# Optimization experiments

Hardware: AMD Instinct MI355X
Metric: run time of the kernel (lower is better)

## Reference

```python
import jax, jax.numpy as jnp
import numpy as np

B, GH, GW = 8, 32, 32
S = GH * GW            # 1024
HIDDEN = 512
D = 64                 # head_dim
NUM_HOPS = 2
EPS = 1e-6


def setup_inputs() -> dict:
    key = jax.random.key(0)
    ks = jax.random.split(key, 8)

    def init(k, shape, std):
        return (jax.random.normal(k, shape) * std).astype(jnp.float32)

    x = jax.random.normal(ks[0], (B, S, HIDDEN), dtype=jnp.float32)
    Wq = init(ks[1], (D, HIDDEN), HIDDEN ** -0.5)
    Wk = init(ks[2], (D, HIDDEN), HIDDEN ** -0.5)
    Wv = init(ks[3], (D, HIDDEN), HIDDEN ** -0.5)
    bias_table = init(ks[4], (2 * GH - 1, 2 * GW - 1), 0.02)
    fusion_w = jnp.ones((NUM_HOPS, 3), dtype=jnp.float32)
    fusion_b = jnp.zeros((NUM_HOPS,), dtype=jnp.float32)
    hop_W = init(ks[5], (NUM_HOPS, D, D), D ** -0.5)
    gate_W = init(ks[6], (NUM_HOPS, HIDDEN), HIDDEN ** -0.5)
    gate_b = jnp.zeros((NUM_HOPS,), dtype=jnp.float32)
    out_W = init(ks[7], (HIDDEN, D), D ** -0.5)
    temperature = jnp.ones((1,), dtype=jnp.float32)

    # relative position index [S, S] (buffer, constant)
    coords = np.stack(np.meshgrid(np.arange(GH), np.arange(GW), indexing='ij')).reshape(2, -1)
    rel = coords[:, :, None] - coords[:, None, :]
    rel[0] += GH - 1
    rel[1] += GW - 1
    rel_idx = jnp.asarray(rel[0] * (2 * GW - 1) + rel[1], dtype=jnp.int32)

    return dict(x=x, Wq=Wq, Wk=Wk, Wv=Wv, bias_table=bias_table,
                fusion_w=fusion_w, fusion_b=fusion_b, hop_W=hop_W,
                gate_W=gate_W, gate_b=gate_b, out_W=out_W,
                temperature=temperature, rel_idx=rel_idx)


def _rotate_half(u):
    d = u.shape[-1] // 2
    return jnp.concatenate([-u[..., d:], u[..., :d]], axis=-1)


def _prob_log(p):
    p = jnp.clip(p, EPS, 1.0 - EPS)
    return jnp.log(p / (1.0 - p + EPS))


def _mat_exp(M, h):
    R = M
    for _ in range(h - 1):
        R = jnp.matmul(R, M)
    return R


def _row_norm(M):
    return M / (jnp.sum(M, axis=-1, keepdims=True) + EPS)


def reference(x, Wq, Wk, Wv, bias_table, fusion_w, fusion_b, hop_W,
              gate_W, gate_b, out_W, temperature, rel_idx):
    b, s, hdim = x.shape
    d = Wq.shape[0]
    n_hops = hop_W.shape[0]
    scale = jnp.sqrt(jnp.float32(d))

    Q = jnp.einsum('bsh,dh->bsd', x, Wq)
    K = jnp.einsum('bsh,dh->bsd', x, Wk)
    V = jnp.einsum('bsh,dh->bsd', x, Wv)

    # RoPE (cached cos/sin are deterministic functions of S, D)
    inv_freq = 1.0 / (10000.0 ** (jnp.arange(0, d, 2, dtype=jnp.float32) / d))
    t = jnp.arange(s, dtype=jnp.float32)
    emb = jnp.concatenate([jnp.outer(t, inv_freq)] * 2, axis=-1)  # [S, D]
    cos, sin = jnp.cos(emb), jnp.sin(emb)
    Q = Q * cos + _rotate_half(Q) * sin
    K = K * cos + _rotate_half(K) * sin

    pb = bias_table.reshape(-1)[rel_idx]  # [S, S]
    scores = (jnp.einsum('bsd,btd->bst', Q, K) / scale + pb[None])
    scores = scores / jnp.clip(temperature, 0.1, None)
    A = jax.nn.softmax(scores, axis=-1)  # [B, S, S]

    A_T = jnp.swapaxes(A, -1, -2)
    AAt = jnp.matmul(A, A_T)
    AtA = jnp.matmul(A_T, A)

    hop_outs = []
    for hop in range(n_hops):
        h = hop + 1
        A_seq = _row_norm(_mat_exp(A, h))
        A_co = _row_norm(_mat_exp(AAt, h))
        A_sp = _row_norm(_mat_exp(AtA, h))
        fused_logit = (fusion_b[hop]
                       + fusion_w[hop, 0] * _prob_log(A_seq)
                       + fusion_w[hop, 1] * _prob_log(A_co)
                       + fusion_w[hop, 2] * _prob_log(A_sp))
        fused = _row_norm(jax.nn.sigmoid(fused_logit))
        hop_v = jnp.einsum('bsd,ed->bse', V, hop_W[hop])
        hop_outs.append(jnp.matmul(fused, hop_v))  # [B, S, D]

    gate = jax.nn.softmax(jnp.einsum('bsh,gh->bsg', x, gate_W) + gate_b, axis=-1)
    combined = sum(hop_outs[i] * gate[..., i:i + 1] for i in range(n_hops))
    return jnp.einsum('bsd,hd->bsh', combined, out_W)
```

## Files before the change

kernel.cpp:

```cpp
#include <hip/hip_runtime.h>
#include <hip/hip_bf16.h>

#define BB 8
#define SS 1024
#define HH 512
#define DD 64

typedef unsigned short u16;
typedef short v8s __attribute__((ext_vector_type(8)));
typedef float v4f __attribute__((ext_vector_type(4)));

__device__ __forceinline__ float bf2f(u16 u) {
    union { unsigned int i; float f; } v; v.i = ((unsigned int)u) << 16; return v.f;
}
__device__ __forceinline__ u16 f2bf(float f) {
    union { float f; unsigned int i; } v; v.f = f;
    unsigned int u = v.i;
    unsigned int r = u + 0x7fffu + ((u >> 16) & 1u);
    return (u16)(r >> 16);
}

__device__ __forceinline__ void gload16(const u16* g, u16* l) {
    __builtin_amdgcn_global_load_lds(
        (const __attribute__((address_space(1))) void*)g,
        (__attribute__((address_space(3))) void*)l,
        16, 0, 0);
}

__device__ __forceinline__ void tile_1024(
    const u16* __restrict__ Xb, const u16* __restrict__ Yb,
    u16* __restrict__ Cd, int tm, int tn, u16* Xs, u16* Ys, int mirror)
{
    int t = threadIdx.x, lane = t & 63, w = t >> 6;
    int wm = (w & 1) << 6, wn = (w >> 1) << 6;
    int fr = lane & 15, q = lane >> 4, m7 = fr & 7;
    int subrow = lane >> 3, cch = (lane & 7) ^ subrow;

    const u16* xg[4]; const u16* yg[4]; u16* xl[4]; u16* yl[4];
    #pragma unroll
    for (int i = 0; i < 4; i++) {
        int r = i * 32 + w * 8 + subrow;
        xg[i] = Xb + (long)(tm + r) * 1024 + cch * 8;
        yg[i] = Yb + (long)(tn + r) * 1024 + cch * 8;
        xl[i] = Xs + (i * 32 + w * 8) * 64;
        yl[i] = Ys + (i * 32 + w * 8) * 64;
    }

    v4f acc[4][4];
    #pragma unroll
    for (int i = 0; i < 4; i++)
        #pragma unroll
        for (int j = 0; j < 4; j++) {
            acc[i][j][0] = 0.f; acc[i][j][1] = 0.f; acc[i][j][2] = 0.f; acc[i][j][3] = 0.f;
        }

    for (int k0 = 0; k0 < 1024; k0 += 64) {
        __syncthreads();
        #pragma unroll
        for (int i = 0; i < 4; i++) { gload16(xg[i] + k0, xl[i]); gload16(yg[i] + k0, yl[i]); }
        __syncthreads();
        v8s af[2][4], bfr[2][4];
        #pragma unroll
        for (int h = 0; h < 2; h++) {
            int ca = (((h << 2) + q) ^ m7) << 3;
            #pragma unroll
            for (int s = 0; s < 4; s++) {
                af[h][s]  = *(const v8s*)(Xs + (wm + s * 16 + fr) * 64 + ca);
                bfr[h][s] = *(const v8s*)(Ys + (wn + s * 16 + fr) * 64 + ca);
            }
        }
        #pragma unroll
        for (int h = 0; h < 2; h++)
            #pragma unroll
            for (int i = 0; i < 4; i++)
                #pragma unroll
                for (int j = 0; j < 4; j++)
                    acc[i][j] = __builtin_amdgcn_mfma_f32_16x16x32_bf16(af[h][i], bfr[h][j], acc[i][j], 0, 0, 0);
    }
    #pragma unroll
    for (int i = 0; i < 4; i++) {
        int rowb = tm + wm + i * 16 + q * 4;
        #pragma unroll
        for (int j = 0; j < 4; j++) {
            int col = tn + wn + j * 16 + fr;
            ushort4 pv;
            pv.x = f2bf(acc[i][j][0]); pv.y = f2bf(acc[i][j][1]);
            pv.z = f2bf(acc[i][j][2]); pv.w = f2bf(acc[i][j][3]);
            #pragma unroll
            for (int r = 0; r < 4; r++)
                Cd[(long)(rowb + r) * 1024 + col] = ((u16*)&pv)[r];
            if (mirror)
                *(ushort4*)(Cd + (long)col * 1024 + rowb) = pv;
        }
    }
}

__device__ __forceinline__ void tile_k64(
    const u16* __restrict__ Xrows, const u16* __restrict__ Yrows,
    void* __restrict__ Cd, int crs, int cf32, u16* Xs, u16* Ys)
{
    int t = threadIdx.x, lane = t & 63, w = t >> 6;
    int wm = (w & 1) << 6, wn = (w >> 1) << 6;
    int fr = lane & 15, q = lane >> 4, m7 = fr & 7;
    int subrow = lane >> 3, cch = (lane & 7) ^ subrow;

    #pragma unroll
    for (int i = 0; i < 4; i++) {
        int r = i * 32 + w * 8 + subrow;
        gload16(Xrows + (long)r * 64 + cch * 8, Xs + (i * 32 + w * 8) * 64);
        gload16(Yrows + (long)r * 64 + cch * 8, Ys + (i * 32 + w * 8) * 64);
    }
    __syncthreads();

    v4f acc[4][4];
    #pragma unroll
    for (int i = 0; i < 4; i++)
        #pragma unroll
        for (int j = 0; j < 4; j++) {
            acc[i][j][0] = 0.f; acc[i][j][1] = 0.f; acc[i][j][2] = 0.f; acc[i][j][3] = 0.f;
        }
    v8s af[2][4], bfr[2][4];
    #pragma unroll
    for (int h = 0; h < 2; h++) {
        int ca = (((h << 2) + q) ^ m7) << 3;
        #pragma unroll
        for (int s = 0; s < 4; s++) {
            af[h][s]  = *(const v8s*)(Xs + (wm + s * 16 + fr) * 64 + ca);
            bfr[h][s] = *(const v8s*)(Ys + (wn + s * 16 + fr) * 64 + ca);
        }
    }
    #pragma unroll
    for (int h = 0; h < 2; h++)
        #pragma unroll
        for (int i = 0; i < 4; i++)
            #pragma unroll
            for (int j = 0; j < 4; j++)
                acc[i][j] = __builtin_amdgcn_mfma_f32_16x16x32_bf16(af[h][i], bfr[h][j], acc[i][j], 0, 0, 0);
    #pragma unroll
    for (int i = 0; i < 4; i++) {
        int rowb = wm + i * 16 + q * 4;
        #pragma unroll
        for (int j = 0; j < 4; j++) {
            int col = wn + j * 16 + fr;
            #pragma unroll
            for (int r = 0; r < 4; r++) {
                long o = (long)(rowb + r) * crs + col;
                if (cf32) ((float*)Cd)[o] = acc[i][j][r];
                else      ((u16*)Cd)[o] = f2bf(acc[i][j][r]);
            }
        }
    }
}

__device__ __forceinline__ void hop_tile(
    const u16* __restrict__ Fb, const u16* __restrict__ Hb,
    int y, int tmt, float* __restrict__ Pd, u16* Fs, u16* Hs)
{
    int tm = tmt * 128, kb = y * 256;
    int t = threadIdx.x, lane = t & 63, w = t >> 6;
    int fr = lane & 15, q = lane >> 4, m7 = fr & 7;
    int subrow = lane >> 3, cch = (lane & 7) ^ subrow;

    const u16* fg[4]; u16* fl[4]; const u16* hg[2]; u16* hl[2];
    #pragma unroll
    for (int i = 0; i < 4; i++) {
        int r = i * 32 + w * 8 + subrow;
        fg[i] = Fb + (long)(tm + r) * 1024 + cch * 8;
        fl[i] = Fs + (i * 32 + w * 8) * 64;
    }
    #pragma unroll
    for (int i = 0; i < 2; i++) {
        int r = i * 32 + w * 8 + subrow;
        hg[i] = Hb + (long)r * 1024 + cch * 8;
        hl[i] = Hs + (i * 32 + w * 8) * 64;
    }

    v4f acc[2][4];
    #pragma unroll
    for (int i = 0; i < 2; i++)
        #pragma unroll
        for (int j = 0; j < 4; j++) {
            acc[i][j][0] = 0.f; acc[i][j][1] = 0.f; acc[i][j][2] = 0.f; acc[i][j][3] = 0.f;
        }

    for (int k0 = kb; k0 < kb + 256; k0 += 64) {
        __syncthreads();
        #pragma unroll
        for (int i = 0; i < 4; i++) gload16(fg[i] + k0, fl[i]);
        #pragma unroll
        for (int i = 0; i < 2; i++) gload16(hg[i] + k0, hl[i]);
        __syncthreads();
        v8s af[2][2], bfr[2][4];
        #pragma unroll
        for (int h = 0; h < 2; h++) {
            int ca = (((h << 2) + q) ^ m7) << 3;
            #pragma unroll
            for (int s = 0; s < 2; s++)
                af[h][s] = *(const v8s*)(Fs + (w * 32 + s * 16 + fr) * 64 + ca);
            #pragma unroll
            for (int s = 0; s < 4; s++)
                bfr[h][s] = *(const v8s*)(Hs + (s * 16 + fr) * 64 + ca);
        }
        #pragma unroll
        for (int h = 0; h < 2; h++)
            #pragma unroll
            for (int i = 0; i < 2; i++)
                #pragma unroll
                for (int j = 0; j < 4; j++)
                    acc[i][j] = __builtin_amdgcn_mfma_f32_16x16x32_bf16(af[h][i], bfr[h][j], acc[i][j], 0, 0, 0);
    }
    #pragma unroll
    for (int i = 0; i < 2; i++) {
        int rowb = tm + w * 32 + i * 16 + q * 4;
        #pragma unroll
        for (int j = 0; j < 4; j++) {
            int col = j * 16 + fr;
            #pragma unroll
            for (int r = 0; r < 4; r++)
                Pd[(long)(rowb + r) * 64 + col] = acc[i][j][r];
        }
    }
}

__device__ __forceinline__ void fused_row(
    const u16* __restrict__ r1, const u16* __restrict__ r2, const u16* __restrict__ r3,
    float w0, float w1, float w2, float b0, u16* __restrict__ Frow, int lane)
{
    int base = lane << 4;
    union U { uint4 v; u16 s[8]; };
    U a[2], b[2], c[2];
    a[0].v = *(const uint4*)(r1 + base); a[1].v = *(const uint4*)(r1 + base + 8);
    b[0].v = *(const uint4*)(r2 + base); b[1].v = *(const uint4*)(r2 + base + 8);
    c[0].v = *(const uint4*)(r3 + base); c[1].v = *(const uint4*)(r3 + base + 8);
    float m1[16], m2[16], m3[16];
    float s1 = 0.f, s2 = 0.f, s3 = 0.f;
    #pragma unroll
    for (int h = 0; h < 2; h++)
        #pragma unroll
        for (int e = 0; e < 8; e++) {
            int k = h * 8 + e;
            m1[k] = bf2f(a[h].s[e]); m2[k] = bf2f(b[h].s[e]); m3[k] = bf2f(c[h].s[e]);
            s1 += m1[k]; s2 += m2[k]; s3 += m3[k];
        }
    #pragma unroll
    for (int o = 1; o < 64; o <<= 1) {
        s1 += __shfl_xor(s1, o); s2 += __shfl_xor(s2, o); s3 += __shfl_xor(s3, o);
    }
    float i1 = 1.f / (s1 + 1e-6f), i2 = 1.f / (s2 + 1e-6f), i3 = 1.f / (s3 + 1e-6f);
    float sig[16];
    float ssum = 0.f;
    #pragma unroll
    for (int k = 0; k < 16; k++) {
        float p1 = fminf(fmaxf(m1[k] * i1, 1e-6f), 1.0f - 1e-6f);
        float p2 = fminf(fmaxf(m2[k] * i2, 1e-6f), 1.0f - 1e-6f);
        float p3 = fminf(fmaxf(m3[k] * i3, 1e-6f), 1.0f - 1e-6f);
        float l1 = __logf(p1 / (1.0f - p1 + 1e-6f));
        float l2 = __logf(p2 / (1.0f - p2 + 1e-6f));
        float l3 = __logf(p3 / (1.0f - p3 + 1e-6f));
        float lg = b0 + w0 * l1 + w1 * l2 + w2 * l3;
        float sg = 1.0f / (1.0f + __expf(-lg));
        sig[k] = sg; ssum += sg;
    }
    #pragma unroll
    for (int o = 1; o < 64; o <<= 1) ssum += __shfl_xor(ssum, o);
    float inv = 1.0f / (ssum + 1e-6f);
    U o0, o1;
    #pragma unroll
    for (int e = 0; e < 8; e++) { o0.s[e] = f2bf(sig[e] * inv); o1.s[e] = f2bf(sig[8 + e] * inv); }
    *(uint4*)(Frow + base) = o0.v;
    *(uint4*)(Frow + base + 8) = o1.v;
}

__global__ __launch_bounds__(256) void gemm_link1(
    const u16* __restrict__ A, const u16* __restrict__ AT,
    u16* __restrict__ AAt, u16* __restrict__ AtA, u16* __restrict__ A2)
{
    __shared__ u16 Xs[128 * 64];
    __shared__ u16 Ys[128 * 64];
    const long SSq = (long)SS * SS;
    int b = blockIdx.x & 7;
    int job = blockIdx.x >> 3;
    const u16* Xb; const u16* Yb; u16* Cd;
    int ti, tj, mir;
    if (job < 72) {
        int tt = job < 36 ? job : job - 36;
        ti = 0;
        while (tt >= 8 - ti) { tt -= 8 - ti; ti++; }
        tj = ti + tt;
        mir = (ti != tj);
        if (job < 36) { Xb = A  + b * SSq; Yb = Xb; Cd = AAt + b * SSq; }
        else          { Xb = AT + b * SSq; Yb = Xb; Cd = AtA + b * SSq; }
    } else {
        int jj = job - 72;
        ti = jj >> 3; tj = jj & 7; mir = 0;
        Xb = A + b * SSq; Yb = AT + b * SSq; Cd = A2 + b * SSq;
    }
    tile_1024(Xb, Yb, Cd, ti * 128, tj * 128, Xs, Ys, mir);
}

__global__ __launch_bounds__(256) void k_link2_fused0(
    const u16* __restrict__ AAt, const u16* __restrict__ AtA,
    u16* __restrict__ AAt2, u16* __restrict__ AtA2,
    const u16* __restrict__ A, const float* __restrict__ fw,
    const float* __restrict__ fbv, u16* __restrict__ F0)
{
    __shared__ u16 Xs[128 * 64];
    __shared__ u16 Ys[128 * 64];
    const long SSq = (long)SS * SS;
    int bx = blockIdx.x;
    if (bx < 576) {
        int z = bx & 15;
        int tt = bx >> 4, ti = 0;
        while (tt >= 8 - ti) { tt -= 8 - ti; ti++; }
        int tj = ti + tt;
        const u16* Xb = (z < 8 ? AAt : AtA) + (long)(z & 7) * SSq;
        u16* Cd = (z < 8 ? AAt2 : AtA2) + (long)(z & 7) * SSq;
        tile_1024(Xb, Xb, Cd, ti * 128, tj * 128, Xs, Ys, ti != tj);
    } else {
        int lane = threadIdx.x & 63, w = threadIdx.x >> 6;
        float w0 = fw[0], w1 = fw[1], w2 = fw[2], b0 = fbv[0];
        long row = (long)(bx - 576) * 4 + w;
        fused_row(A + row * 1024, AAt + row * 1024, AtA + row * 1024,
                  w0, w1, w2, b0, F0 + row * 1024, lane);
    }
}

__global__ __launch_bounds__(256) void k_hop0_fused1(
    const u16* __restrict__ F0, const u16* __restrict__ hopVT,
    float* __restrict__ Pa, float* __restrict__ Pb,
    const u16* __restrict__ A2, const u16* __restrict__ AAt2,
    const u16* __restrict__ AtA2, const float* __restrict__ fw,
    const float* __restrict__ fbv, u16* __restrict__ F1)
{
    __shared__ u16 Fs[128 * 64];
    __shared__ u16 Hs[64 * 64];
    const long SSq = (long)SS * SS;
    int bx = blockIdx.x;
    if (bx < 256) {
        int y = bx >> 6, rest = bx & 63;
        int tmt = rest >> 3, b = rest & 7;
        float* Pd = (y < 2 ? Pa + (long)y * 16 * 65536 : Pb + (long)(y - 2) * 16 * 65536)
                    + (long)b * 65536;
        hop_tile(F0 + (long)b * SSq, hopVT + (long)b * 65536, y, tmt, Pd, Fs, Hs);
    } else {
        int lane = threadIdx.x & 63, w = threadIdx.x >> 6;
        float w0 = fw[3], w1 = fw[4], w2 = fw[5], b0 = fbv[1];
        long row = (long)(bx - 256) * 4 + w;
        fused_row(A2 + row * 1024, AAt2 + row * 1024, AtA2 + row * 1024,
                  w0, w1, w2, b0, F1 + row * 1024, lane);
    }
}

__global__ __launch_bounds__(256) void gemm_hop1(
    const u16* __restrict__ F1, const u16* __restrict__ hopVT,
    float* __restrict__ Pa, float* __restrict__ Pb)
{
    __shared__ u16 Fs[128 * 64];
    __shared__ u16 Hs[64 * 64];
    const long SSq = (long)SS * SS;
    int j = blockIdx.x;
    int y = j >> 6, rest = j & 63;
    int tmt = rest >> 3, b = rest & 7;
    float* Pd = (y < 2 ? Pa + (long)y * 16 * 65536 : Pb + (long)(y - 2) * 16 * 65536)
                + (long)(8 + b) * 65536;
    hop_tile(F1 + (long)b * SSq, hopVT + (long)(8 + b) * 65536, y, tmt, Pd, Fs, Hs);
}

__global__ __launch_bounds__(256) void gemm_nt(
    const u16* __restrict__ X, long sx,
    const u16* __restrict__ Y, long sy,
    void* __restrict__ Cv, long sc,
    int M, int N, int K, int cf32)
{
    __shared__ u16 Xs[128 * 64];
    __shared__ u16 Ys[128 * 64];
    const u16* Xb = X + (long)blockIdx.z * sx;
    const u16* Yb = Y + (long)blockIdx.z * sy;
    int tm = blockIdx.x * 128, tn = blockIdx.y * 128;
    int t = threadIdx.x, lane = t & 63, w = t >> 6;
    int wm = (w & 1) << 6, wn = (w >> 1) << 6;
    int fr = lane & 15, q = lane >> 4, m7 = fr & 7;
    int subrow = lane >> 3, cch = (lane & 7) ^ subrow;

    const u16* xg[4]; const u16* yg[4]; u16* xl[4]; u16* yl[4];
    #pragma unroll
    for (int i = 0; i < 4; i++) {
        int r = i * 32 + w * 8 + subrow;
        xg[i] = Xb + (long)(tm + r) * K + cch * 8;
        yg[i] = Yb + (long)(tn + r) * K + cch * 8;
        xl[i] = Xs + (i * 32 + w * 8) * 64;
        yl[i] = Ys + (i * 32 + w * 8) * 64;
    }

    v4f acc[4][4];
    #pragma unroll
    for (int i = 0; i < 4; i++)
        #pragma unroll
        for (int j = 0; j < 4; j++) {
            acc[i][j][0] = 0.f; acc[i][j][1] = 0.f; acc[i][j][2] = 0.f; acc[i][j][3] = 0.f;
        }

    for (int k0 = 0; k0 < K; k0 += 64) {
        __syncthreads();
        #pragma unroll
        for (int i = 0; i < 4; i++) { gload16(xg[i] + k0, xl[i]); gload16(yg[i] + k0, yl[i]); }
        __syncthreads();
        v8s af[2][4], bfr[2][4];
        #pragma unroll
        for (int h = 0; h < 2; h++) {
            int ca = (((h << 2) + q) ^ m7) << 3;
            #pragma unroll
            for (int s = 0; s < 4; s++) {
                af[h][s]  = *(const v8s*)(Xs + (wm + s * 16 + fr) * 64 + ca);
                bfr[h][s] = *(const v8s*)(Ys + (wn + s * 16 + fr) * 64 + ca);
            }
        }
        #pragma unroll
        for (int h = 0; h < 2; h++)
            #pragma unroll
            for (int i = 0; i < 4; i++)
                #pragma unroll
                for (int j = 0; j < 4; j++)
                    acc[i][j] = __builtin_amdgcn_mfma_f32_16x16x32_bf16(af[h][i], bfr[h][j], acc[i][j], 0, 0, 0);
    }
    long cb = (long)blockIdx.z * sc;
    #pragma unroll
    for (int i = 0; i < 4; i++) {
        int rowb = tm + wm + i * 16 + q * 4;
        #pragma unroll
        for (int j = 0; j < 4; j++) {
            int col = tn + wn + j * 16 + fr;
            #pragma unroll
            for (int r = 0; r < 4; r++) {
                long o = cb + (long)(rowb + r) * N + col;
                if (cf32) ((float*)Cv)[o] = acc[i][j][r];
                else      ((u16*)Cv)[o] = f2bf(acc[i][j][r]);
            }
        }
    }
}

__global__ __launch_bounds__(256) void k_proj_rope(
    const u16* __restrict__ xb, const u16* __restrict__ wpack,
    const float* __restrict__ gateb, const float2* __restrict__ ropetab,
    u16* __restrict__ Qb, u16* __restrict__ Kb, u16* __restrict__ Vb,
    float* __restrict__ gate)
{
    __shared__ u16 Xs[128 * 64];
    __shared__ u16 Ys[128 * 64];
    int tm = blockIdx.x * 128, tn = blockIdx.y * 128;
    int t = threadIdx.x, lane = t & 63, w = t >> 6;
    int wm = (w & 1) << 6, wn = (w >> 1) << 6;
    int fr = lane & 15, q = lane >> 4, m7 = fr & 7;
    int subrow = lane >> 3, cch = (lane & 7) ^ subrow;

    const u16* xg[4]; const u16* yg[4]; u16* xl[4]; u16* yl[4];
    #pragma unroll
    for (int i = 0; i < 4; i++) {
        int r = i * 32 + w * 8 + subrow;
        xg[i] = xb + (long)(tm + r) * 512 + cch * 8;
        yg[i] = wpack + (long)(tn + r) * 512 + cch * 8;
        xl[i] = Xs + (i * 32 + w * 8) * 64;
        yl[i] = Ys + (i * 32 + w * 8) * 64;
    }

    v4f acc[4][4];
    #pragma unroll
    for (int i = 0; i < 4; i++)
        #pragma unroll
        for (int j = 0; j < 4; j++) {
            acc[i][j][0] = 0.f; acc[i][j][1] = 0.f; acc[i][j][2] = 0.f; acc[i][j][3] = 0.f;
        }

    for (int k0 = 0; k0 < 512; k0 += 64) {
        __syncthreads();
        #pragma unroll
        for (int i = 0; i < 4; i++) { gload16(xg[i] + k0, xl[i]); gload16(yg[i] + k0, yl[i]); }
        __syncthreads();
        v8s af[2][4], bfr[2][4];
        #pragma unroll
        for (int h = 0; h < 2; h++) {
            int ca = (((h << 2) + q) ^ m7) << 3;
            #pragma unroll
            for (int s = 0; s < 4; s++) {
                af[h][s]  = *(const v8s*)(Xs + (wm + s * 16 + fr) * 64 + ca);
                bfr[h][s] = *(const v8s*)(Ys + (wn + s * 16 + fr) * 64 + ca);
            }
        }
        #pragma unroll
        for (int h = 0; h < 2; h++)
            #pragma unroll
            for (int i = 0; i < 4; i++)
                #pragma unroll
                for (int j = 0; j < 4; j++)
                    acc[i][j] = __builtin_amdgcn_mfma_f32_16x16x32_bf16(af[h][i], bfr[h][j], acc[i][j], 0, 0, 0);
    }

    if (blockIdx.y == 0) {
        u16* dst = wn ? Kb : Qb;
        #pragma unroll
        for (int i = 0; i < 4; i++) {
            #pragma unroll
            for (int r = 0; r < 4; r++) {
                int row = tm + wm + i * 16 + q * 4 + r;
                int spos = row & (SS - 1);
                float2 t0 = ropetab[spos * 32 + fr];
                float2 t1 = ropetab[spos * 32 + 16 + fr];
                #pragma unroll
                for (int j = 0; j < 4; j++) {
                    float v = acc[i][j][r], p = acc[i][j ^ 2][r];
                    float cs = (j & 1) ? t1.x : t0.x;
                    float sn = (j & 1) ? t1.y : t0.y;
                    float o = (j & 2) ? (v * cs + p * sn) : (v * cs - p * sn);
                    dst[(long)row * 64 + j * 16 + fr] = f2bf(o);
                }
            }
        }
    } else if (wn == 0) {
        #pragma unroll
        for (int i = 0; i < 4; i++)
            #pragma unroll
            for (int j = 0; j < 4; j++)
                #pragma unroll
                for (int r = 0; r < 4; r++) {
                    int row = tm + wm + i * 16 + q * 4 + r;
                    Vb[(long)row * 64 + j * 16 + fr] = f2bf(acc[i][j][r]);
                }
    } else {
        float gb = gateb[fr & 1];
        #pragma unroll
        for (int i = 0; i < 4; i++)
            #pragma unroll
            for (int r = 0; r < 4; r++) {
                int row = tm + wm + i * 16 + q * 4 + r;
                float g = acc[i][0][r] + gb;
                float go = __shfl_xor(g, 1);
                float m = fmaxf(g, go);
                float e = __expf(g - m), eo = __expf(go - m);
                if (fr < 2) gate[(long)row * 2 + fr] = e / (e + eo);
            }
    }
}

__global__ __launch_bounds__(256) void k_qk_hopv(
    const u16* __restrict__ Qb, const u16* __restrict__ Kb,
    const u16* __restrict__ Vb, const u16* __restrict__ hopWb,
    float* __restrict__ scores, u16* __restrict__ hopvC)
{
    __shared__ u16 Xs[128 * 64];
    __shared__ u16 Ys[128 * 64];
    const long SSq = (long)SS * SS;
    const long SD = (long)SS * DD;
    int bx = blockIdx.x;
    if (bx < 512) {
        int z = bx & 7;
        int tt = bx >> 3;
        int tm = (tt >> 3) * 128, tn = (tt & 7) * 128;
        tile_k64(Qb + z * SD + (long)tm * 64, Kb + z * SD + (long)tn * 64,
                 scores + z * SSq + (long)tm * 1024 + tn, 1024, 1, Xs, Ys);
    } else {
        int tm = (bx - 512) * 128;
        tile_k64(Vb + (long)tm * 64, hopWb,
                 hopvC + (long)tm * 128, 128, 0, Xs, Ys);
    }
}

__global__ __launch_bounds__(256) void k_sm_hvt(
    const float* __restrict__ scores, const float* __restrict__ btab,
    const float* __restrict__ temp, u16* __restrict__ A,
    u16* __restrict__ AT,
    const u16* __restrict__ hopvC, u16* __restrict__ hopVT)
{
    __shared__ __align__(16) float smf[3969];
    __shared__ __align__(8) u16 Atile[4096];
    int bx = blockIdx.x;
    int t = threadIdx.x;
    if (bx < 2048) {
        for (int i = t; i < 3969; i += 256) smf[i] = btab[i];
        __syncthreads();
        int lane = t & 63, w = t >> 6;
        long row = (long)bx * 4 + w;
        int i = (int)(row & 1023);
        int ih = i >> 5, iw = i & 31;
        float inv_t = 1.0f / fmaxf(temp[0], 0.1f);
        const float* srow = scores + row * 1024;
        float sc[16];
        float m = -1e30f;
        #pragma unroll
        for (int c = 0; c < 16; c++) {
            int j = c * 64 + lane;
            int jh = j >> 5, jw = j & 31;
            float pb = smf[(ih - jh + 31) * 63 + (iw - jw + 31)];
            float s = (srow[j] * 0.125f + pb) * inv_t;
            sc[c] = s; m = fmaxf(m, s);
        }
        #pragma unroll
        for (int o = 1; o < 64; o <<= 1) m = fmaxf(m, __shfl_xor(m, o));
        float sum = 0.f;
        #pragma unroll
        for (int c = 0; c < 16; c++) { sc[c] = __expf(sc[c] - m); sum += sc[c]; }
        #pragma unroll
        for (int o = 1; o < 64; o <<= 1) sum += __shfl_xor(sum, o);
        float inv = 1.0f / sum;
        #pragma unroll
        for (int c = 0; c < 16; c++) {
            u16 bv = f2bf(sc[c] * inv);
            A[row * 1024 + c * 64 + lane] = bv;
            Atile[w * 1024 + c * 64 + lane] = bv;
        }
        __syncthreads();
        int row0 = bx * 4;
        int bb = row0 >> 10;
        int i0 = row0 & 1023;
        u16* ATb = AT + (long)bb * ((long)SS * SS);
        #pragma unroll
        for (int k = 0; k < 4; k++) {
            int col = k * 256 + t;
            ushort4 ov;
            ov.x = Atile[col];        ov.y = Atile[1024 + col];
            ov.z = Atile[2048 + col]; ov.w = Atile[3072 + col];
            *(ushort4*)(ATb + (long)col * 1024 + i0) = ov;
        }
    } else {
        u16* tile = (u16*)smf;
        int ex = bx - 2048;
        int hop = ex >> 7, rem = ex & 127;
        int z = rem & 7, i0 = (rem >> 3) * 64;
        const u16* s = hopvC + (long)z * (1024 * 128) + hop * 64;
        u16* d = hopVT + (long)(hop * 8 + z) * 65536;
        int r = t >> 2, c0 = (t & 3) << 4;
        #pragma unroll
        for (int p = 0; p < 2; p++) {
            int c = c0 + p * 8;
            uint4 v = *(const uint4*)(s + (long)(i0 + r) * 128 + c);
            *(uint4*)(&tile[r * 72 + c]) = v;
        }
        __syncthreads();
        #pragma unroll
        for (int p = 0; p < 2; p++) {
            uint4 ov; u16* po = (u16*)&ov;
            #pragma unroll
            for (int e = 0; e < 8; e++) po[e] = tile[(c0 + p * 8 + e) * 72 + r];
            *(uint4*)(d + (long)r * 1024 + i0 + c0 + p * 8) = ov;
        }
    }
}

__global__ __launch_bounds__(256) void k_pack(
    const float* __restrict__ x, const float* __restrict__ Wq,
    const float* __restrict__ Wk, const float* __restrict__ Wv,
    const float* __restrict__ gW, const float* __restrict__ hopW,
    const float* __restrict__ outW, u16* __restrict__ xb,
    u16* __restrict__ wpack, u16* __restrict__ hopWb, u16* __restrict__ outWb,
    float2* __restrict__ ropetab)
{
    int bx = blockIdx.x;
    if (bx < 4096) {
        long i = (long)bx * 256 + threadIdx.x;
        float4 v = ((const float4*)x)[i];
        ushort4 o;
        o.x = f2bf(v.x); o.y = f2bf(v.y); o.z = f2bf(v.z); o.w = f2bf(v.w);
        ((ushort4*)xb)[i] = o;
    } else if (bx < 4768) {
        int idx = (bx - 4096) * 256 + threadIdx.x;
        if (idx < 131072) {
            int r = idx >> 9, c = idx & 511;
            float v = 0.f;
            if (r < 64)       v = Wq[r * 512 + c];
            else if (r < 128) v = Wk[(r - 64) * 512 + c];
            else if (r < 192) v = Wv[(r - 128) * 512 + c];
            else if (r < 194) v = gW[(r - 192) * 512 + c];
            wpack[idx] = f2bf(v);
        } else if (idx < 131072 + 8192) {
            int i = idx - 131072;
            hopWb[i] = f2bf(hopW[i]);
        } else if (idx < 131072 + 8192 + 32768) {
            int i = idx - 131072 - 8192;
            outWb[i] = f2bf(outW[i]);
        }
    } else {
        int idx = (bx - 4768) * 256 + threadIdx.x;
        int spos = idx >> 5, f = idx & 31;
        float ang = (float)spos * exp2f(-(float)f * (13.287712379549449f / 32.0f));
        float sn, cs;
        sincosf(ang, &sn, &cs);
        ropetab[idx] = make_float2(cs, sn);
    }
}

__global__ __launch_bounds__(256) void k_combine(
    const float* __restrict__ Pa, const float* __restrict__ Pb,
    const float* __restrict__ gate, u16* __restrict__ comb)
{
    long idx = (long)blockIdx.x * 256 + threadIdx.x;
    long srow = idx >> 6;
    int b = (int)(srow >> 10);
    long o = (long)(srow & 1023) * 64 + (idx & 63);
    float h0 = Pa[(long)b * 65536 + o] + Pa[(long)(16 + b) * 65536 + o]
             + Pb[(long)b * 65536 + o] + Pb[(long)(16 + b) * 65536 + o];
    float h1 = Pa[(long)(8 + b) * 65536 + o] + Pa[(long)(24 + b) * 65536 + o]
             + Pb[(long)(8 + b) * 65536 + o] + Pb[(long)(24 + b) * 65536 + o];
    float g0 = gate[srow * 2], g1 = gate[srow * 2 + 1];
    comb[idx] = f2bf(h0 * g0 + h1 * g1);
}

extern "C" void kernel_launch(void* const* d_in, const int* in_sizes, int n_in,
                              void* d_out, int out_size, void* d_ws, size_t ws_size,
                              hipStream_t stream) {
    const float* x    = (const float*)d_in[0];
    const float* Wq   = (const float*)d_in[1];
    const float* Wk   = (const float*)d_in[2];
    const float* Wv   = (const float*)d_in[3];
    const float* btab = (const float*)d_in[4];
    const float* fw   = (const float*)d_in[5];
    const float* fbv  = (const float*)d_in[6];
    const float* hopW = (const float*)d_in[7];
    const float* gW   = (const float*)d_in[8];
    const float* gb   = (const float*)d_in[9];
    const float* outW = (const float*)d_in[10];
    const float* temp = (const float*)d_in[11];
    float* out = (float*)d_out;

    char* wsb = (char*)d_ws;
    size_t off = 0;
    auto take = [&](size_t n) { char* p = wsb + off; off += (n + 255) & ~(size_t)255; return p; };
    u16* Qb      = (u16*)take(8192L * 64 * 2);
    u16* Kb      = (u16*)take(8192L * 64 * 2);
    u16* Vb      = (u16*)take(8192L * 64 * 2);
    float* gate  = (float*)take(8192L * 2 * 4);
    u16* wpack   = (u16*)take(256L * 512 * 2);
    u16* hopWb   = (u16*)take(2L * 64 * 64 * 2);
    u16* outWb   = (u16*)take(512L * 64 * 2);
    float2* ropetab = (float2*)take(1024L * 32 * 8);
    u16* hopvC   = (u16*)take(8192L * 128 * 2);
    u16* hopVT   = (u16*)take(2L * 8 * 64 * 1024 * 2);
    float* Pa    = (float*)take(2L * 16 * 65536 * 4);
    u16* comb    = (u16*)take(8192L * 64 * 2);
    float* scoresF = (float*)take(8L * 1024 * 1024 * 4);
    u16* F0      = (u16*)scoresF;
    u16* F1      = (u16*)scoresF + 8L * 1024 * 1024;
    u16* A       = (u16*)take(8L * 1024 * 1024 * 2);
    u16* xb      = (u16*)A;
    u16* AT      = (u16*)take(8L * 1024 * 1024 * 2);
    float* Pb    = (float*)AT;
    u16* AAt     = (u16*)take(8L * 1024 * 1024 * 2);
    u16* AtA     = (u16*)take(8L * 1024 * 1024 * 2);
    u16* A2      = (u16*)take(8L * 1024 * 1024 * 2);
    u16* AAt2    = (u16*)take(8L * 1024 * 1024 * 2);
    u16* AtA2    = (u16*)take(8L * 1024 * 1024 * 2);
    (void)ws_size; (void)in_sizes; (void)n_in; (void)out_size;

    k_pack<<<4896, 256, 0, stream>>>(x, Wq, Wk, Wv, gW, hopW, outW, xb, wpack,
                                     hopWb, outWb, ropetab);
    k_proj_rope<<<dim3(64, 2, 1), 256, 0, stream>>>(xb, wpack, gb, ropetab,
                                                    Qb, Kb, Vb, gate);
    k_qk_hopv<<<576, 256, 0, stream>>>(Qb, Kb, Vb, hopWb, scoresF, hopvC);
    k_sm_hvt<<<2304, 256, 0, stream>>>(scoresF, btab, temp, A, AT, hopvC, hopVT);
    gemm_link1<<<1088, 256, 0, stream>>>(A, AT, AAt, AtA, A2);
    k_link2_fused0<<<2624, 256, 0, stream>>>(AAt, AtA, AAt2, AtA2, A, fw, fbv, F0);
    k_hop0_fused1<<<2304, 256, 0, stream>>>(F0, hopVT, Pa, Pb, A2, AAt2, AtA2,
                                            fw, fbv, F1);
    gemm_hop1<<<256, 256, 0, stream>>>(F1, hopVT, Pa, Pb);
    k_combine<<<2048, 256, 0, stream>>>(Pa, Pb, gate, comb);
    gemm_nt<<<dim3(64, 4, 1), 256, 0, stream>>>(comb, 0, outWb, 0, out, 0, 8192, 512, 64, 1);
}
```

Baseline: 301.7 us.

## Fuse QK^T scores with softmax and fold hop-V projection into link1 GEMM

Replaces the separate QK^T GEMM (which wrote fp32 scores) and the softmax/transpose kernel with a single kernel. It computes each 16-row block of scores via MFMA in registers, adds the relative position bias, exponentiates, reduces row sums and writes A and A^T directly. The hop-V projection now runs as extra blocks of gemm_link1 and writes the transposed hopVT layout directly, dropping the hopvC intermediate and the transpose pass. This removes a 32MB fp32 round trip and one launch. The softmax skips max subtraction, so it relies on scores staying small, and K rows are read from global memory without LDS tiling.

```diff
diff --git a/kernel.cpp b/kernel.cpp
--- a/kernel.cpp
+++ b/kernel.cpp
@@ -95,9 +95,9 @@
     }
 }
 
-__device__ __forceinline__ void tile_k64(
-    const u16* __restrict__ Xrows, const u16* __restrict__ Yrows,
-    void* __restrict__ Cd, int crs, int cf32, u16* Xs, u16* Ys)
+__device__ __forceinline__ void hopv_tile(
+    const u16* __restrict__ Vrows, const u16* __restrict__ Hw,
+    u16* __restrict__ hopVT, int tm, u16* Xs, u16* Ys)
 {
     int t = threadIdx.x, lane = t & 63, w = t >> 6;
     int wm = (w & 1) << 6, wn = (w >> 1) << 6;
@@ -107,8 +107,8 @@
     #pragma unroll
     for (int i = 0; i < 4; i++) {
         int r = i * 32 + w * 8 + subrow;
-        gload16(Xrows + (long)r * 64 + cch * 8, Xs + (i * 32 + w * 8) * 64);
-        gload16(Yrows + (long)r * 64 + cch * 8, Ys + (i * 32 + w * 8) * 64);
+        gload16(Vrows + (long)(tm + r) * 64 + cch * 8, Xs + (i * 32 + w * 8) * 64);
+        gload16(Hw + (long)r * 64 + cch * 8, Ys + (i * 32 + w * 8) * 64);
     }
     __syncthreads();
 
@@ -136,18 +136,19 @@
             #pragma unroll
             for (int j = 0; j < 4; j++)
                 acc[i][j] = __builtin_amdgcn_mfma_f32_16x16x32_bf16(af[h][i], bfr[h][j], acc[i][j], 0, 0, 0);
+
+    int z = tm >> 10, sb = tm & 1023;
     #pragma unroll
     for (int i = 0; i < 4; i++) {
         int rowb = wm + i * 16 + q * 4;
         #pragma unroll
         for (int j = 0; j < 4; j++) {
-            int col = wn + j * 16 + fr;
-            #pragma unroll
-            for (int r = 0; r < 4; r++) {
-                long o = (long)(rowb + r) * crs + col;
-                if (cf32) ((float*)Cd)[o] = acc[i][j][r];
-                else      ((u16*)Cd)[o] = f2bf(acc[i][j][r]);
-            }
+            int colY = wn + j * 16 + fr;
+            int hop = colY >> 6, e = colY & 63;
+            ushort4 pv;
+            pv.x = f2bf(acc[i][j][0]); pv.y = f2bf(acc[i][j][1]);
+            pv.z = f2bf(acc[i][j][2]); pv.w = f2bf(acc[i][j][3]);
+            *(ushort4*)(hopVT + (long)(hop * 8 + z) * 65536 + (long)e * 1024 + sb + rowb) = pv;
         }
     }
 }
@@ -271,13 +272,102 @@
     *(uint4*)(Frow + base + 8) = o1.v;
 }
 
+__global__ __launch_bounds__(256) void k_qksm(
+    const u16* __restrict__ Qb, const u16* __restrict__ Kb,
+    const float* __restrict__ btab, const float* __restrict__ temp,
+    u16* __restrict__ A, u16* __restrict__ AT)
+{
+    __shared__ __align__(16) float smf[3969];
+    __shared__ float lred[4][16];
+    int t = threadIdx.x, lane = t & 63, w = t >> 6;
+    int fr = lane & 15, q4 = lane >> 4;
+    int bx = blockIdx.x;
+    int z = bx >> 6;
+    int rb = (bx & 63) << 4;
+    for (int i = t; i < 3969; i += 256) smf[i] = btab[i];
+    __syncthreads();
+    float invt = 1.0f / fmaxf(temp[0], 0.1f);
+    const long SD = (long)SS * DD;
+    const long SSq = (long)SS * SS;
+    const u16* qrow = Qb + (long)z * SD + (long)(rb + fr) * 64 + q4 * 8;
+    v8s aq0 = *(const v8s*)(qrow);
+    v8s aq1 = *(const v8s*)(qrow + 32);
+    int ih[4], iw[4];
+    #pragma unroll
+    for (int r = 0; r < 4; r++) {
+        int ii = rb + q4 * 4 + r;
+        ih[r] = ii >> 5; iw[r] = ii & 31;
+    }
+    const u16* kb0 = Kb + (long)z * SD + q4 * 8;
+    int c0 = w << 8;
+    float ef[16][4];
+    float l0 = 0.f, l1 = 0.f, l2 = 0.f, l3 = 0.f;
+    #pragma unroll
+    for (int f = 0; f < 16; f++) {
+        int colK = c0 + f * 16 + fr;
+        const u16* krow = kb0 + (long)colK * 64;
+        v8s bk0 = *(const v8s*)(krow);
+        v8s bk1 = *(const v8s*)(krow + 32);
+        v4f acc = {0.f, 0.f, 0.f, 0.f};
+        acc = __builtin_amdgcn_mfma_f32_16x16x32_bf16(aq0, bk0, acc, 0, 0, 0);
+        acc = __builtin_amdgcn_mfma_f32_16x16x32_bf16(aq1, bk1, acc, 0, 0, 0);
+        int jh = colK >> 5, jw = colK & 31;
+        #pragma unroll
+        for (int r = 0; r < 4; r++) {
+            float pb = smf[(ih[r] - jh + 31) * 63 + (iw[r] - jw + 31)];
+            float s = (acc[r] * 0.125f + pb) * invt;
+            float e = __expf(s);
+            ef[f][r] = e;
+            if (r == 0) l0 += e; else if (r == 1) l1 += e;
+            else if (r == 2) l2 += e; else l3 += e;
+        }
+    }
+    #pragma unroll
+    for (int o = 1; o < 16; o <<= 1) {
+        l0 += __shfl_xor(l0, o); l1 += __shfl_xor(l1, o);
+        l2 += __shfl_xor(l2, o); l3 += __shfl_xor(l3, o);
+    }
+    if (fr == 0) {
+        lred[w][q4 * 4 + 0] = l0; lred[w][q4 * 4 + 1] = l1;
+        lred[w][q4 * 4 + 2] = l2; lred[w][q4 * 4 + 3] = l3;
+    }
+    __syncthreads();
+    float invl[4];
+    #pragma unroll
+    for (int r = 0; r < 4; r++) {
+        int idx = q4 * 4 + r;
+        invl[r] = 1.0f / (lred[0][idx] + lred[1][idx] + lred[2][idx] + lred[3][idx]);
+    }
+    u16* Ab = A + (long)z * SSq;
+    u16* ATb = AT + (long)z * SSq;
+    #pragma unroll
+    for (int f = 0; f < 16; f++) {
+        int colK = c0 + f * 16 + fr;
+        ushort4 pv;
+        u16* pp = (u16*)&pv;
+        #pragma unroll
+        for (int r = 0; r < 4; r++) {
+            u16 bv = f2bf(ef[f][r] * invl[r]);
+            pp[r] = bv;
+            Ab[(long)(rb + q4 * 4 + r) * 1024 + colK] = bv;
+        }
+        *(ushort4*)(ATb + (long)colK * 1024 + rb + q4 * 4) = pv;
+    }
+}
+
 __global__ __launch_bounds__(256) void gemm_link1(
     const u16* __restrict__ A, const u16* __restrict__ AT,
-    u16* __restrict__ AAt, u16* __restrict__ AtA, u16* __restrict__ A2)
+    u16* __restrict__ AAt, u16* __restrict__ AtA, u16* __restrict__ A2,
+    const u16* __restrict__ Vb, const u16* __restrict__ hopWb,
+    u16* __restrict__ hopVT)
 {
     __shared__ u16 Xs[128 * 64];
     __shared__ u16 Ys[128 * 64];
     const long SSq = (long)SS * SS;
+    if (blockIdx.x >= 1088) {
+        hopv_tile(Vb, hopWb, hopVT, (blockIdx.x - 1088) * 128, Xs, Ys);
+        return;
+    }
     int b = blockIdx.x & 7;
     int job = blockIdx.x >> 3;
     const u16* Xb; const u16* Yb; u16* Cd;
@@ -539,110 +629,6 @@
                 float e = __expf(g - m), eo = __expf(go - m);
                 if (fr < 2) gate[(long)row * 2 + fr] = e / (e + eo);
             }
-    }
-}
-
-__global__ __launch_bounds__(256) void k_qk_hopv(
-    const u16* __restrict__ Qb, const u16* __restrict__ Kb,
-    const u16* __restrict__ Vb, const u16* __restrict__ hopWb,
-    float* __restrict__ scores, u16* __restrict__ hopvC)
-{
-    __shared__ u16 Xs[128 * 64];
-    __shared__ u16 Ys[128 * 64];
-    const long SSq = (long)SS * SS;
-    const long SD = (long)SS * DD;
-    int bx = blockIdx.x;
-    if (bx < 512) {
-        int z = bx & 7;
-        int tt = bx >> 3;
-        int tm = (tt >> 3) * 128, tn = (tt & 7) * 128;
-        tile_k64(Qb + z * SD + (long)tm * 64, Kb + z * SD + (long)tn * 64,
-                 scores + z * SSq + (long)tm * 1024 + tn, 1024, 1, Xs, Ys);
-    } else {
-        int tm = (bx - 512) * 128;
-        tile_k64(Vb + (long)tm * 64, hopWb,
-                 hopvC + (long)tm * 128, 128, 0, Xs, Ys);
-    }
-}
-
-__global__ __launch_bounds__(256) void k_sm_hvt(
-    const float* __restrict__ scores, const float* __restrict__ btab,
-    const float* __restrict__ temp, u16* __restrict__ A,
-    u16* __restrict__ AT,
-    const u16* __restrict__ hopvC, u16* __restrict__ hopVT)
-{
-    __shared__ __align__(16) float smf[3969];
-    __shared__ __align__(8) u16 Atile[4096];
-    int bx = blockIdx.x;
-    int t = threadIdx.x;
-    if (bx < 2048) {
-        for (int i = t; i < 3969; i += 256) smf[i] = btab[i];
-        __syncthreads();
-        int lane = t & 63, w = t >> 6;
-        long row = (long)bx * 4 + w;
-        int i = (int)(row & 1023);
-        int ih = i >> 5, iw = i & 31;
-        float inv_t = 1.0f / fmaxf(temp[0], 0.1f);
-        const float* srow = scores + row * 1024;
-        float sc[16];
-        float m = -1e30f;
-        #pragma unroll
-        for (int c = 0; c < 16; c++) {
-            int j = c * 64 + lane;
-            int jh = j >> 5, jw = j & 31;
-            float pb = smf[(ih - jh + 31) * 63 + (iw - jw + 31)];
-            float s = (srow[j] * 0.125f + pb) * inv_t;
-            sc[c] = s; m = fmaxf(m, s);
-        }
-        #pragma unroll
-        for (int o = 1; o < 64; o <<= 1) m = fmaxf(m, __shfl_xor(m, o));
-        float sum = 0.f;
-        #pragma unroll
-        for (int c = 0; c < 16; c++) { sc[c] = __expf(sc[c] - m); sum += sc[c]; }
-        #pragma unroll
-        for (int o = 1; o < 64; o <<= 1) sum += __shfl_xor(sum, o);
-        float inv = 1.0f / sum;
-        #pragma unroll
-        for (int c = 0; c < 16; c++) {
-            u16 bv = f2bf(sc[c] * inv);
-            A[row * 1024 + c * 64 + lane] = bv;
-            Atile[w * 1024 + c * 64 + lane] = bv;
-        }
-        __syncthreads();
-        int row0 = bx * 4;
-        int bb = row0 >> 10;
-        int i0 = row0 & 1023;
-        u16* ATb = AT + (long)bb * ((long)SS * SS);
-        #pragma unroll
-        for (int k = 0; k < 4; k++) {
-            int col = k * 256 + t;
-            ushort4 ov;
-            ov.x = Atile[col];        ov.y = Atile[1024 + col];
-            ov.z = Atile[2048 + col]; ov.w = Atile[3072 + col];
-            *(ushort4*)(ATb + (long)col * 1024 + i0) = ov;
-        }
-    } else {
-        u16* tile = (u16*)smf;
-        int ex = bx - 2048;
-        int hop = ex >> 7, rem = ex & 127;
-        int z = rem & 7, i0 = (rem >> 3) * 64;
-        const u16* s = hopvC + (long)z * (1024 * 128) + hop * 64;
-        u16* d = hopVT + (long)(hop * 8 + z) * 65536;
-        int r = t >> 2, c0 = (t & 3) << 4;
-        #pragma unroll
-        for (int p = 0; p < 2; p++) {
-            int c = c0 + p * 8;
-            uint4 v = *(const uint4*)(s + (long)(i0 + r) * 128 + c);
-            *(uint4*)(&tile[r * 72 + c]) = v;
-        }
-        __syncthreads();
-        #pragma unroll
-        for (int p = 0; p < 2; p++) {
-            uint4 ov; u16* po = (u16*)&ov;
-            #pragma unroll
-            for (int e = 0; e < 8; e++) po[e] = tile[(c0 + p * 8 + e) * 72 + r];
-            *(uint4*)(d + (long)r * 1024 + i0 + c0 + p * 8) = ov;
-        }
     }
 }
 
@@ -732,13 +718,12 @@
     u16* hopWb   = (u16*)take(2L * 64 * 64 * 2);
     u16* outWb   = (u16*)take(512L * 64 * 2);
     float2* ropetab = (float2*)take(1024L * 32 * 8);
-    u16* hopvC   = (u16*)take(8192L * 128 * 2);
     u16* hopVT   = (u16*)take(2L * 8 * 64 * 1024 * 2);
     float* Pa    = (float*)take(2L * 16 * 65536 * 4);
     u16* comb    = (u16*)take(8192L * 64 * 2);
-    float* scoresF = (float*)take(8L * 1024 * 1024 * 4);
-    u16* F0      = (u16*)scoresF;
-    u16* F1      = (u16*)scoresF + 8L * 1024 * 1024;
+    char* fregion = take(8L * 1024 * 1024 * 4);
+    u16* F0      = (u16*)fregion;
+    u16* F1      = (u16*)fregion + 8L * 1024 * 1024;
     u16* A       = (u16*)take(8L * 1024 * 1024 * 2);
     u16* xb      = (u16*)A;
     u16* AT      = (u16*)take(8L * 1024 * 1024 * 2);
@@ -754,9 +739,8 @@
                                      hopWb, outWb, ropetab);
     k_proj_rope<<<dim3(64, 2, 1), 256, 0, stream>>>(xb, wpack, gb, ropetab,
                                                     Qb, Kb, Vb, gate);
-    k_qk_hopv<<<576, 256, 0, stream>>>(Qb, Kb, Vb, hopWb, scoresF, hopvC);
-    k_sm_hvt<<<2304, 256, 0, stream>>>(scoresF, btab, temp, A, AT, hopvC, hopVT);
-    gemm_link1<<<1088, 256, 0, stream>>>(A, AT, AAt, AtA, A2);
+    k_qksm<<<512, 256, 0, stream>>>(Qb, Kb, btab, temp, A, AT);
+    gemm_link1<<<1152, 256, 0, stream>>>(A, AT, AAt, AtA, A2, Vb, hopWb, hopVT);
     k_link2_fused0<<<2624, 256, 0, stream>>>(AAt, AtA, AAt2, AtA2, A, fw, fbv, F0);
     k_hop0_fused1<<<2304, 256, 0, stream>>>(F0, hopVT, Pa, Pb, A2, AAt2, AtA2,
                                             fw, fbv, F1);
```

Result: faster. 276.8 us (-8.2%).
